# Performance work log

Hardware: AMD Instinct MI355X
Metric: run time of the kernel (lower is better)

The kernel has to match this reference:

```python
import jax, jax.numpy as jnp
import numpy as np

N = 100000
E = 3200000
F_IN, H1, H2, C = 256, 64, 32, 1000


def setup_inputs() -> dict:
    key = jax.random.key(0)
    ks = jax.random.split(key, 10)
    x = jax.random.normal(ks[0], (N, F_IN), dtype=jnp.float32)
    edge_src = jax.random.randint(ks[1], (E,), 0, N, dtype=jnp.int32)
    edge_dst = jax.random.randint(ks[2], (E,), 0, N, dtype=jnp.int32)
    s1 = 1.0 / np.sqrt(F_IN)
    s2 = 1.0 / np.sqrt(H1)
    s3 = 1.0 / np.sqrt(H2)
    W1 = jax.random.uniform(ks[3], (F_IN, H1), jnp.float32, -s1, s1)
    b1 = jnp.zeros((H1,), jnp.float32)
    W2 = jax.random.uniform(ks[4], (H1, H2), jnp.float32, -s2, s2)
    b2 = jnp.zeros((H2,), jnp.float32)
    Wfc = jax.random.uniform(ks[5], (H2, C), jnp.float32, -s3, s3)
    bfc = jax.random.uniform(ks[6], (C,), jnp.float32, -s3, s3)
    return {"x": x, "edge_src": edge_src, "edge_dst": edge_dst,
            "W1": W1, "b1": b1, "W2": W2, "b2": b2, "Wfc": Wfc, "bfc": bfc}


def _gcn_conv(x, W, b, src, dst, dinv):
    # PyG GCNConv: linear transform, then normalized scatter-add (with self-loops).
    xw = x @ W  # [N, out]
    coef = dinv[src] * dinv[dst]  # [E]
    msg = xw[src] * coef[:, None]  # gathered, scaled messages
    agg = jax.ops.segment_sum(msg, dst, num_segments=x.shape[0])
    agg = agg + xw * (dinv * dinv)[:, None]  # self-loop contribution
    return agg + b


def reference(x, edge_src, edge_dst, W1, b1, W2, b2, Wfc, bfc):
    n = x.shape[0]
    # degree with self-loops, counted on target nodes
    deg = 1.0 + jax.ops.segment_sum(jnp.ones_like(edge_dst, dtype=x.dtype), edge_dst, num_segments=n)
    dinv = jax.lax.rsqrt(deg)
    h = jax.nn.relu(_gcn_conv(x, W1, b1, edge_src, edge_dst, dinv))
    h = jax.nn.relu(_gcn_conv(h, W2, b2, edge_src, edge_dst, dinv))
    g = jnp.mean(h, axis=0)  # [H2]
    return g @ Wfc + bfc  # [C]
```

## Files before the change

kernel.cpp:

```cpp
#include <hip/hip_runtime.h>

#define N_NODES 100000
#define N_EDGES 3200000
#define F_IN 256
#define H1 64
#define H2 32
#define C_OUT 1000

#define OFF_G     0
#define OFF_DINV  64
#define OFF_CNT   100096
#define OFF_HEAD  200128
#define OFF_NODE2 300160
#define OFF_Y1B   6700160
#define OFF_Y2Q   9900160

__device__ __forceinline__ unsigned short f2bf(float f) {
    unsigned u = __float_as_uint(f);
    u += 0x7FFFu + ((u >> 16) & 1u);
    return (unsigned short)(u >> 16);
}
__device__ __forceinline__ float bf2f(unsigned short s) {
    return __uint_as_float(((unsigned)s) << 16);
}

__device__ __forceinline__ unsigned char f2fp8(float x) {
    x = fminf(fmaxf(x, -448.0f), 448.0f);
    unsigned u = __float_as_uint(x);
    unsigned s = (u >> 24) & 0x80u;
    unsigned absu = u & 0x7fffffffu;
    float ax = __uint_as_float(absu);
    if (ax < 0.015625f) {
        int q = __float2int_rn(ax * 512.0f);
        return (unsigned char)(s | (unsigned)q);
    }
    int e = (int)(absu >> 23) - 127;
    unsigned man = absu & 0x7fffffu;
    unsigned m3 = man >> 20;
    unsigned rem = man & 0xFFFFFu;
    if (rem > 0x80000u || (rem == 0x80000u && (m3 & 1u))) m3++;
    if (m3 == 8u) { m3 = 0u; e++; }
    if (e > 8) return (unsigned char)(s | 0x7Eu);
    return (unsigned char)(s | ((unsigned)(e + 7) << 3) | m3);
}

__device__ __forceinline__ float fp8lut_val(int t) {
    int ex = (t >> 3) & 15, man = t & 7;
    int base = ex ? (8 + man) : man;
    float v = ldexpf((float)base, (ex ? ex : 1) - 10);
    return (t & 0x80) ? -v : v;
}

__global__ void k_init(int* __restrict__ head, int* __restrict__ cnt,
                       float* __restrict__ g) {
    int i = blockIdx.x * 256 + threadIdx.x;
    if (i < N_NODES) { head[i] = -1; cnt[i] = 0; }
    if (blockIdx.x == 0 && threadIdx.x < H2) g[threadIdx.x] = 0.0f;
}

__global__ void k_build(const int* __restrict__ src, const int* __restrict__ dst,
                        int* __restrict__ head, int* __restrict__ cnt,
                        int2* __restrict__ node2) {
    int e = blockIdx.x * 256 + threadIdx.x;
    if (e < N_EDGES) {
        int d = dst[e];
        int s = src[e];
        int prev = atomicExch(&head[d], e);
        node2[e] = make_int2(s, prev);
        atomicAdd(&cnt[d], 1);
    }
}

__global__ void k_dinv(const int* __restrict__ cnt, float* __restrict__ dinv) {
    int n = blockIdx.x * 256 + threadIdx.x;
    if (n < N_NODES) dinv[n] = rsqrtf(1.0f + (float)cnt[n]);
}

__global__ __launch_bounds__(256) void k_gemm1(const float* __restrict__ x,
                                               const float* __restrict__ W1,
                                               const float* __restrict__ dinv,
                                               unsigned short* __restrict__ y1b) {
    __shared__ float w[F_IN][H1];
    {
        const float4* Wv = (const float4*)W1;
        float4* wv = (float4*)&w[0][0];
        for (int i = threadIdx.x; i < F_IN * H1 / 4; i += 256) wv[i] = Wv[i];
    }
    __syncthreads();
    int n0 = blockIdx.x * 512 + threadIdx.x;
    int n1 = n0 + 256;
    bool v0 = n0 < N_NODES, v1 = n1 < N_NODES;
    int n0c = v0 ? n0 : 0, n1c = v1 ? n1 : 0;

    float acc0[H1], acc1[H1];
#pragma unroll
    for (int j = 0; j < H1; j++) { acc0[j] = 0.0f; acc1[j] = 0.0f; }

    const float4* xr0 = (const float4*)(x + (size_t)n0c * F_IN);
    const float4* xr1 = (const float4*)(x + (size_t)n1c * F_IN);
#pragma unroll 2
    for (int k0 = 0; k0 < F_IN / 4; k0++) {
        float4 xa = xr0[k0];
        float4 xb = xr1[k0];
#pragma unroll
        for (int d = 0; d < 4; d++) {
            float xv0 = (d == 0 ? xa.x : d == 1 ? xa.y : d == 2 ? xa.z : xa.w);
            float xv1 = (d == 0 ? xb.x : d == 1 ? xb.y : d == 2 ? xb.z : xb.w);
            const float4* wr = (const float4*)&w[k0 * 4 + d][0];
#pragma unroll
            for (int j4 = 0; j4 < H1 / 4; j4++) {
                float4 wq = wr[j4];
                acc0[j4 * 4 + 0] += xv0 * wq.x;
                acc0[j4 * 4 + 1] += xv0 * wq.y;
                acc0[j4 * 4 + 2] += xv0 * wq.z;
                acc0[j4 * 4 + 3] += xv0 * wq.w;
                acc1[j4 * 4 + 0] += xv1 * wq.x;
                acc1[j4 * 4 + 1] += xv1 * wq.y;
                acc1[j4 * 4 + 2] += xv1 * wq.z;
                acc1[j4 * 4 + 3] += xv1 * wq.w;
            }
        }
    }
    if (v0) {
        float dv = dinv[n0];
        unsigned pk[H1 / 2];
#pragma unroll
        for (int j2 = 0; j2 < H1 / 2; j2++) {
            unsigned lo = f2bf(acc0[2 * j2] * dv);
            unsigned hi = f2bf(acc0[2 * j2 + 1] * dv);
            pk[j2] = lo | (hi << 16);
        }
        uint4* o = (uint4*)(y1b + (size_t)n0 * H1);
#pragma unroll
        for (int q = 0; q < H1 / 8; q++)
            o[q] = make_uint4(pk[q * 4], pk[q * 4 + 1], pk[q * 4 + 2], pk[q * 4 + 3]);
    }
    if (v1) {
        float dv = dinv[n1];
        unsigned pk[H1 / 2];
#pragma unroll
        for (int j2 = 0; j2 < H1 / 2; j2++) {
            unsigned lo = f2bf(acc1[2 * j2] * dv);
            unsigned hi = f2bf(acc1[2 * j2 + 1] * dv);
            pk[j2] = lo | (hi << 16);
        }
        uint4* o = (uint4*)(y1b + (size_t)n1 * H1);
#pragma unroll
        for (int q = 0; q < H1 / 8; q++)
            o[q] = make_uint4(pk[q * 4], pk[q * 4 + 1], pk[q * 4 + 2], pk[q * 4 + 3]);
    }
}

__global__ __launch_bounds__(256) void k_agg1_gemm2(const unsigned short* __restrict__ y1b,
                                                    const int* __restrict__ head,
                                                    const int2* __restrict__ node2,
                                                    const float* __restrict__ dinv,
                                                    const float* __restrict__ b1,
                                                    const float* __restrict__ W2,
                                                    unsigned char* __restrict__ y2q) {
    __shared__ float w2s[H1][H2];
    __shared__ float hbuf[8][H1];
    {
        const float4* Wv = (const float4*)W2;
        float4* wv = (float4*)&w2s[0][0];
        for (int i = threadIdx.x; i < H1 * H2 / 4; i += 256) wv[i] = Wv[i];
    }

    const int t = threadIdx.x;
    const int wid = t >> 6;
    const int c = t & 63;
    const int n0 = blockIdx.x * 8 + wid * 2;
    const int n1 = n0 + 1;

    float a0 = bf2f(y1b[(size_t)n0 * H1 + c]);
    float a1 = bf2f(y1b[(size_t)n1 * H1 + c]);
    int e0 = head[n0], e1 = head[n1];
    while (e0 >= 0 && e1 >= 0) {
        int2 v0 = node2[e0];
        int2 v1 = node2[e1];
        a0 += bf2f(y1b[(size_t)v0.x * H1 + c]);
        a1 += bf2f(y1b[(size_t)v1.x * H1 + c]);
        e0 = v0.y; e1 = v1.y;
    }
    while (e0 >= 0) {
        int2 v0 = node2[e0];
        a0 += bf2f(y1b[(size_t)v0.x * H1 + c]);
        e0 = v0.y;
    }
    while (e1 >= 0) {
        int2 v1 = node2[e1];
        a1 += bf2f(y1b[(size_t)v1.x * H1 + c]);
        e1 = v1.y;
    }
    float h0 = dinv[n0] * a0 + b1[c];
    float h1v = dinv[n1] * a1 + b1[c];
    hbuf[wid * 2 + 0][c] = h0 > 0.0f ? h0 : 0.0f;
    hbuf[wid * 2 + 1][c] = h1v > 0.0f ? h1v : 0.0f;
    __syncthreads();

    {
        int w = t >> 5, j = t & 31;
        int n2 = blockIdx.x * 8 + w;
        float dot = 0.0f;
#pragma unroll
        for (int cc = 0; cc < H1; cc++) dot += hbuf[w][cc] * w2s[cc][j];
        y2q[(size_t)n2 * H2 + j] = f2fp8(dinv[n2] * dot);
    }
}

__global__ __launch_bounds__(256) void k_agg2_pool(const unsigned char* __restrict__ y2q,
                                                   const int* __restrict__ head,
                                                   const int2* __restrict__ node2,
                                                   const float* __restrict__ dinv,
                                                   const float* __restrict__ b2,
                                                   float* __restrict__ g) {
    __shared__ float lut[256];
    __shared__ float red[256];
    const int t = threadIdx.x;
    lut[t] = fp8lut_val(t);
    __syncthreads();

    const int n = blockIdx.x * 8 + (t >> 5);
    const int c = t & 31;

    float a = lut[y2q[(size_t)n * H2 + c]];
    int e = head[n];
    while (e >= 0) {
        int2 v = node2[e];
        a += lut[y2q[(size_t)v.x * H2 + c]];
        e = v.y;
    }
    float hv = dinv[n] * a + b2[c];
    red[t] = hv > 0.0f ? hv : 0.0f;
    __syncthreads();
    if (t < 128) red[t] += red[t + 128];
    __syncthreads();
    if (t < 64) red[t] += red[t + 64];
    __syncthreads();
    if (t < 32) {
        float s = red[t] + red[t + 32];
        atomicAdd(&g[t], s);
    }
}

__global__ void k_fc(const float* __restrict__ g, const float* __restrict__ Wfc,
                     const float* __restrict__ bfc, float* __restrict__ out) {
    int c = blockIdx.x * 256 + threadIdx.x;
    if (c < C_OUT) {
        const float invn = 1.0f / (float)N_NODES;
        float s = bfc[c];
#pragma unroll
        for (int k = 0; k < H2; k++) s += (g[k] * invn) * Wfc[k * C_OUT + c];
        out[c] = s;
    }
}

extern "C" void kernel_launch(void* const* d_in, const int* in_sizes, int n_in,
                              void* d_out, int out_size, void* d_ws, size_t ws_size,
                              hipStream_t stream) {
    const float* x   = (const float*)d_in[0];
    const int* esrc  = (const int*)d_in[1];
    const int* edst  = (const int*)d_in[2];
    const float* W1  = (const float*)d_in[3];
    const float* b1  = (const float*)d_in[4];
    const float* W2  = (const float*)d_in[5];
    const float* b2  = (const float*)d_in[6];
    const float* Wfc = (const float*)d_in[7];
    const float* bfc = (const float*)d_in[8];
    float* out = (float*)d_out;

    float* ws = (float*)d_ws;
    float* g    = ws + OFF_G;
    float* dinv = ws + OFF_DINV;
    int*   cnt  = (int*)(ws + OFF_CNT);
    int*   head = (int*)(ws + OFF_HEAD);
    int2*  node2 = (int2*)(ws + OFF_NODE2);
    unsigned short* y1b = (unsigned short*)(ws + OFF_Y1B);
    unsigned char*  y2q = (unsigned char*)(ws + OFF_Y2Q);

    const int nb_n = (N_NODES + 255) / 256;
    const int nb_e = (N_EDGES + 255) / 256;

    k_init<<<nb_n, 256, 0, stream>>>(head, cnt, g);
    k_build<<<nb_e, 256, 0, stream>>>(esrc, edst, head, cnt, node2);
    k_dinv<<<nb_n, 256, 0, stream>>>(cnt, dinv);

    k_gemm1<<<(N_NODES + 511) / 512, 256, 0, stream>>>(x, W1, dinv, y1b);
    k_agg1_gemm2<<<N_NODES / 8, 256, 0, stream>>>(y1b, head, node2, dinv, b1, W2, y2q);
    k_agg2_pool<<<N_NODES / 8, 256, 0, stream>>>(y2q, head, node2, dinv, b2, g);

    k_fc<<<(C_OUT + 255) / 256, 256, 0, stream>>>(g, Wfc, bfc, out);
}
```

Measured before the change: 969.9 us.

## Pack head and count into one 64-bit CAS and build CSR for layer two

The edge build now updates a packed 64-bit word per node (count plus list head) with a CAS loop, replacing the separate atomicExch and atomicAdd. A single-block prefix scan computes per-node offsets, and the first aggregation pass writes the neighbor ids it walks into a CSR array. The second aggregation then iterates contiguous CSR ranges instead of chasing the linked list, removing its dependent loads. The costs are CAS retries on contended nodes, a serial single-block scan, and extra writes of the CSR array during layer one.

```diff
diff --git a/kernel.cpp b/kernel.cpp
--- a/kernel.cpp
+++ b/kernel.cpp
@@ -7,13 +7,16 @@
 #define H2 32
 #define C_OUT 1000
 
-#define OFF_G     0
-#define OFF_DINV  64
-#define OFF_CNT   100096
-#define OFF_HEAD  200128
-#define OFF_NODE2 300160
-#define OFF_Y1B   6700160
-#define OFF_Y2Q   9900160
+#define OFF_PACKED 0
+#define OFF_G      200000
+#define OFF_DINV   200064
+#define OFF_CNT    300160
+#define OFF_HEAD   400256
+#define OFF_OFS    500352
+#define OFF_CSR    600448
+#define OFF_NODE2  3800448
+#define OFF_Y1B    10200448
+#define OFF_Y2Q    13400448
 
 __device__ __forceinline__ unsigned short f2bf(float f) {
     unsigned u = __float_as_uint(f);
@@ -51,29 +54,68 @@
     return (t & 0x80) ? -v : v;
 }
 
-__global__ void k_init(int* __restrict__ head, int* __restrict__ cnt,
-                       float* __restrict__ g) {
+__global__ void k_init(unsigned long long* __restrict__ packed, float* __restrict__ g) {
     int i = blockIdx.x * 256 + threadIdx.x;
-    if (i < N_NODES) { head[i] = -1; cnt[i] = 0; }
+    if (i < N_NODES) packed[i] = 0ULL;
     if (blockIdx.x == 0 && threadIdx.x < H2) g[threadIdx.x] = 0.0f;
 }
 
 __global__ void k_build(const int* __restrict__ src, const int* __restrict__ dst,
-                        int* __restrict__ head, int* __restrict__ cnt,
+                        unsigned long long* __restrict__ packed,
                         int2* __restrict__ node2) {
     int e = blockIdx.x * 256 + threadIdx.x;
     if (e < N_EDGES) {
         int d = dst[e];
         int s = src[e];
-        int prev = atomicExch(&head[d], e);
-        node2[e] = make_int2(s, prev);
-        atomicAdd(&cnt[d], 1);
-    }
-}
-
-__global__ void k_dinv(const int* __restrict__ cnt, float* __restrict__ dinv) {
+        unsigned long long* addr = &packed[d];
+        unsigned long long old = *addr;
+        for (;;) {
+            unsigned long long nv =
+                (((old >> 32) + 1ULL) << 32) | (unsigned long long)(unsigned)(e + 1);
+            unsigned long long got = atomicCAS(addr, old, nv);
+            if (got == old) break;
+            old = got;
+        }
+        node2[e] = make_int2(s, (int)(unsigned)(old & 0xffffffffULL) - 1);
+    }
+}
+
+__global__ void k_dinv(const unsigned long long* __restrict__ packed,
+                       int* __restrict__ cnt, int* __restrict__ head,
+                       float* __restrict__ dinv) {
     int n = blockIdx.x * 256 + threadIdx.x;
-    if (n < N_NODES) dinv[n] = rsqrtf(1.0f + (float)cnt[n]);
+    if (n < N_NODES) {
+        unsigned long long p = packed[n];
+        int cdeg = (int)(p >> 32);
+        cnt[n] = cdeg;
+        head[n] = (int)(unsigned)(p & 0xffffffffULL) - 1;
+        dinv[n] = rsqrtf(1.0f + (float)cdeg);
+    }
+}
+
+__global__ __launch_bounds__(1024) void k_scan(const int* __restrict__ cnt,
+                                               int* __restrict__ ofs) {
+    __shared__ int lds[1024];
+    const int t = threadIdx.x;
+    const int CH = (N_NODES + 1023) / 1024;
+    int base = t * CH;
+    int end = base + CH; if (end > N_NODES) end = N_NODES;
+    int s = 0;
+    for (int i = base; i < end; i++) s += cnt[i];
+    lds[t] = s;
+    __syncthreads();
+    for (int off = 1; off < 1024; off <<= 1) {
+        int v = (t >= off) ? lds[t - off] : 0;
+        __syncthreads();
+        lds[t] += v;
+        __syncthreads();
+    }
+    int run = lds[t] - s;
+    for (int i = base; i < end; i++) {
+        ofs[i] = run;
+        run += cnt[i];
+    }
+    if (t == 1023) ofs[N_NODES] = lds[1023];
 }
 
 __global__ __launch_bounds__(256) void k_gemm1(const float* __restrict__ x,
@@ -154,6 +196,8 @@
 __global__ __launch_bounds__(256) void k_agg1_gemm2(const unsigned short* __restrict__ y1b,
                                                     const int* __restrict__ head,
                                                     const int2* __restrict__ node2,
+                                                    const int* __restrict__ ofs,
+                                                    int* __restrict__ csr,
                                                     const float* __restrict__ dinv,
                                                     const float* __restrict__ b1,
                                                     const float* __restrict__ W2,
@@ -168,29 +212,37 @@
 
     const int t = threadIdx.x;
     const int wid = t >> 6;
-    const int c = t & 63;
+    const int lane = t & 63;
+    const int c = lane;
     const int n0 = blockIdx.x * 8 + wid * 2;
     const int n1 = n0 + 1;
 
     float a0 = bf2f(y1b[(size_t)n0 * H1 + c]);
     float a1 = bf2f(y1b[(size_t)n1 * H1 + c]);
     int e0 = head[n0], e1 = head[n1];
+    const int ofs0 = ofs[n0], ofs1 = ofs[n1];
+    int k = 0;
     while (e0 >= 0 && e1 >= 0) {
         int2 v0 = node2[e0];
         int2 v1 = node2[e1];
+        if (lane == 0) csr[ofs0 + k] = v0.x;
+        if (lane == 1) csr[ofs1 + k] = v1.x;
         a0 += bf2f(y1b[(size_t)v0.x * H1 + c]);
         a1 += bf2f(y1b[(size_t)v1.x * H1 + c]);
-        e0 = v0.y; e1 = v1.y;
-    }
+        e0 = v0.y; e1 = v1.y; k++;
+    }
+    int k0 = k, k1 = k;
     while (e0 >= 0) {
         int2 v0 = node2[e0];
+        if (lane == 0) csr[ofs0 + k0] = v0.x;
         a0 += bf2f(y1b[(size_t)v0.x * H1 + c]);
-        e0 = v0.y;
+        e0 = v0.y; k0++;
     }
     while (e1 >= 0) {
         int2 v1 = node2[e1];
+        if (lane == 1) csr[ofs1 + k1] = v1.x;
         a1 += bf2f(y1b[(size_t)v1.x * H1 + c]);
-        e1 = v1.y;
+        e1 = v1.y; k1++;
     }
     float h0 = dinv[n0] * a0 + b1[c];
     float h1v = dinv[n1] * a1 + b1[c];
@@ -209,8 +261,8 @@
 }
 
 __global__ __launch_bounds__(256) void k_agg2_pool(const unsigned char* __restrict__ y2q,
-                                                   const int* __restrict__ head,
-                                                   const int2* __restrict__ node2,
+                                                   const int* __restrict__ ofs,
+                                                   const int* __restrict__ csr,
                                                    const float* __restrict__ dinv,
                                                    const float* __restrict__ b2,
                                                    float* __restrict__ g) {
@@ -224,11 +276,10 @@
     const int c = t & 31;
 
     float a = lut[y2q[(size_t)n * H2 + c]];
-    int e = head[n];
-    while (e >= 0) {
-        int2 v = node2[e];
-        a += lut[y2q[(size_t)v.x * H2 + c]];
-        e = v.y;
+    const int p0 = ofs[n], p1 = ofs[n + 1];
+    for (int p = p0; p < p1; p++) {
+        int s = csr[p];
+        a += lut[y2q[(size_t)s * H2 + c]];
     }
     float hv = dinv[n] * a + b2[c];
     red[t] = hv > 0.0f ? hv : 0.0f;
@@ -270,10 +321,13 @@
     float* out = (float*)d_out;
 
     float* ws = (float*)d_ws;
+    unsigned long long* packed = (unsigned long long*)(ws + OFF_PACKED);
     float* g    = ws + OFF_G;
     float* dinv = ws + OFF_DINV;
     int*   cnt  = (int*)(ws + OFF_CNT);
     int*   head = (int*)(ws + OFF_HEAD);
+    int*   ofs  = (int*)(ws + OFF_OFS);
+    int*   csr  = (int*)(ws + OFF_CSR);
     int2*  node2 = (int2*)(ws + OFF_NODE2);
     unsigned short* y1b = (unsigned short*)(ws + OFF_Y1B);
     unsigned char*  y2q = (unsigned char*)(ws + OFF_Y2Q);
@@ -281,13 +335,14 @@
     const int nb_n = (N_NODES + 255) / 256;
     const int nb_e = (N_EDGES + 255) / 256;
 
-    k_init<<<nb_n, 256, 0, stream>>>(head, cnt, g);
-    k_build<<<nb_e, 256, 0, stream>>>(esrc, edst, head, cnt, node2);
-    k_dinv<<<nb_n, 256, 0, stream>>>(cnt, dinv);
+    k_init<<<nb_n, 256, 0, stream>>>(packed, g);
+    k_build<<<nb_e, 256, 0, stream>>>(esrc, edst, packed, node2);
+    k_dinv<<<nb_n, 256, 0, stream>>>(packed, cnt, head, dinv);
+    k_scan<<<1, 1024, 0, stream>>>(cnt, ofs);
 
     k_gemm1<<<(N_NODES + 511) / 512, 256, 0, stream>>>(x, W1, dinv, y1b);
-    k_agg1_gemm2<<<N_NODES / 8, 256, 0, stream>>>(y1b, head, node2, dinv, b1, W2, y2q);
-    k_agg2_pool<<<N_NODES / 8, 256, 0, stream>>>(y2q, head, node2, dinv, b2, g);
+    k_agg1_gemm2<<<N_NODES / 8, 256, 0, stream>>>(y1b, head, node2, ofs, csr, dinv, b1, W2, y2q);
+    k_agg2_pool<<<N_NODES / 8, 256, 0, stream>>>(y2q, ofs, csr, dinv, b2, g);
 
     k_fc<<<(C_OUT + 255) / 256, 256, 0, stream>>>(g, Wfc, bfc, out);
 }
```

After: 1.241 ms. +28.0%, slower.
